# Optimization experiments

Hardware: AMD Instinct MI355X
Metric: run time of the kernel (lower is better)

## Reference

```python
import jax, jax.numpy as jnp
import numpy as np

E = 800_000
D = 64
N_NODES = 50_000


def setup_inputs() -> dict:
    key = jax.random.key(0)
    k1, k2, k3 = jax.random.split(key, 3)
    M = jax.random.normal(k1, (E, D), dtype=jnp.float32)
    edge_index = jax.random.randint(k2, (2, E), 0, N_NODES, dtype=jnp.int64)
    rev_index = jax.random.randint(k3, (E,), 0, E, dtype=jnp.int64)
    return {"M": M, "edge_index": edge_index, "rev_index": rev_index, "dim_size": N_NODES}


def reference(M, edge_index, rev_index, dim_size):
    # directed=True sum-aggregation variant of Aggregation.forward
    src, dest = edge_index[0], edge_index[1]
    # gather: scatter-add edge messages into destination nodes -> [dim_size, D]
    M_v = jax.ops.segment_sum(M, dest, num_segments=dim_size)
    # edge-wise gather by src node, minus reverse-edge message
    return M_v[src] - M[rev_index]
```

## Files before the change

### kernel.cpp

```cpp
#include <hip/hip_runtime.h>


#define D 64
#define N_NODES 50000
#define SCAN_THREADS 1024

__global__ void agg_hist(const int* __restrict__ dest, int* __restrict__ counts, int E) {
    int e = blockIdx.x * blockDim.x + threadIdx.x;
    if (e < E) atomicAdd(counts + dest[e], 1);
}

__global__ void agg_scan(int* __restrict__ data) {
    __shared__ int sums[SCAN_THREADS];
    const int N = N_NODES;
    int t = threadIdx.x;
    const int chunk = (N + SCAN_THREADS - 1) / SCAN_THREADS;
    int start = t * chunk;
    int end   = min(start + chunk, N);
    int s = 0;
    for (int i = start; i < end; ++i) s += data[i];
    sums[t] = s;
    __syncthreads();
    for (int off = 1; off < SCAN_THREADS; off <<= 1) {
        int v = sums[t];
        int u = (t >= off) ? sums[t - off] : 0;
        __syncthreads();
        sums[t] = v + u;
        __syncthreads();
    }
    int run = (t == 0) ? 0 : sums[t - 1];
    for (int i = start; i < end; ++i) {
        int c = data[i];
        data[i] = run;
        run += c;
    }
    if (t == SCAN_THREADS - 1) data[N] = run;
}

__global__ void agg_bin(const int* __restrict__ dest, int* __restrict__ cursor,
                        int* __restrict__ order, int E) {
    int e = blockIdx.x * blockDim.x + threadIdx.x;
    if (e < E) {
        int pos = atomicAdd(cursor + dest[e], 1);
        order[pos] = e;
    }
}

__global__ void agg_reduce(const float* __restrict__ M,
                           const int* __restrict__ order,
                           const int* __restrict__ offsets,
                           float* __restrict__ Mv) {
    int lane = threadIdx.x & 63;
    int node = (blockIdx.x * blockDim.x + threadIdx.x) >> 6;
    if (node >= N_NODES) return;
    int beg = offsets[node];
    int end = offsets[node + 1];
    float acc = 0.f;
    int i = beg;
    for (; i + 4 <= end; i += 4) {
        int e0 = order[i];
        int e1 = order[i + 1];
        int e2 = order[i + 2];
        int e3 = order[i + 3];
        float a0 = M[(size_t)e0 * D + lane];
        float a1 = M[(size_t)e1 * D + lane];
        float a2 = M[(size_t)e2 * D + lane];
        float a3 = M[(size_t)e3 * D + lane];
        acc += (a0 + a1) + (a2 + a3);
    }
    for (; i < end; ++i) acc += M[(size_t)order[i] * D + lane];
    Mv[(size_t)node * D + lane] = acc;
}

__global__ void agg_gather(const float* __restrict__ Mv,
                           const float* __restrict__ M,
                           const int* __restrict__ src,
                           const int* __restrict__ rev,
                           float* __restrict__ out,
                           int E) {
    int gid = blockIdx.x * blockDim.x + threadIdx.x;
    int e  = gid >> 4;
    int c4 = gid & 15;
    if (e >= E) return;
    int s = src[e];
    int r = rev[e];
    float4 a = reinterpret_cast<const float4*>(Mv + (size_t)s * D)[c4];
    float4 b = reinterpret_cast<const float4*>(M  + (size_t)r * D)[c4];
    float4 o;
    o.x = a.x - b.x;
    o.y = a.y - b.y;
    o.z = a.z - b.z;
    o.w = a.w - b.w;
    reinterpret_cast<float4*>(out + (size_t)e * D)[c4] = o;
}

extern "C" void kernel_launch(void* const* d_in, const int* in_sizes, int n_in,
                              void* d_out, int out_size, void* d_ws, size_t ws_size,
                              hipStream_t stream) {
    const float* M   = (const float*)d_in[0];
    const int*   ei  = (const int*)d_in[1];
    const int*   rev = (const int*)d_in[2];

    int E = in_sizes[0] / D;
    const int* src  = ei;
    const int* dest = ei + E;

    int*   offsets = (int*)d_ws;
    int*   cursor  = offsets + 50304;
    int*   order   = cursor + 50304;
    float* Mv      = (float*)(order + 800128);

    hipMemsetAsync(offsets, 0, (N_NODES + 1) * sizeof(int), stream);

    int eb = (E + 255) / 256;
    agg_hist<<<eb, 256, 0, stream>>>(dest, offsets, E);
    agg_scan<<<1, SCAN_THREADS, 0, stream>>>(offsets);
    hipMemcpyAsync(cursor, offsets, (N_NODES + 1) * sizeof(int),
                   hipMemcpyDeviceToDevice, stream);
    agg_bin<<<eb, 256, 0, stream>>>(dest, cursor, order, E);

    int rb = (N_NODES * 64 + 255) / 256;
    agg_reduce<<<rb, 256, 0, stream>>>(M, order, offsets, Mv);

    int gb = (E * 16 + 255) / 256;
    agg_gather<<<gb, 256, 0, stream>>>(Mv, M, src, rev, (float*)d_out, E);
}
```

Measured before the change: 581.5 us.

## Vectorize hist/bin, coalesced warp-shuffle scan writing cursor, unroll reduce, nontemporal stores

The histogram and binning kernels now process four edges per thread using int4 loads. The single-block scan becomes a coalesced, tiled wavefront-shuffle scan that also writes the cursor array, which removes the device-to-device memcpy. The reduce loop is unrolled to eight loads with four independent accumulators to expose more memory-level parallelism. The gather writes its output with nontemporal stores. Together these target launch overhead, the serial uncoalesced scan, and memory latency, at the cost of fewer threads in the atomic kernels and a different floating-point summation order.

```diff
diff --git a/kernel.cpp b/kernel.cpp
--- a/kernel.cpp
+++ b/kernel.cpp
@@ -5,44 +5,73 @@
 #define N_NODES 50000
 #define SCAN_THREADS 1024
 
+typedef float f4 __attribute__((ext_vector_type(4)));
+
 __global__ void agg_hist(const int* __restrict__ dest, int* __restrict__ counts, int E) {
-    int e = blockIdx.x * blockDim.x + threadIdx.x;
-    if (e < E) atomicAdd(counts + dest[e], 1);
+    int t = blockIdx.x * blockDim.x + threadIdx.x;
+    int e = t << 2;
+    if (e + 3 < E) {
+        int4 d = *reinterpret_cast<const int4*>(dest + e);
+        atomicAdd(counts + d.x, 1);
+        atomicAdd(counts + d.y, 1);
+        atomicAdd(counts + d.z, 1);
+        atomicAdd(counts + d.w, 1);
+    } else {
+        for (; e < E; ++e) atomicAdd(counts + dest[e], 1);
+    }
 }
 
-__global__ void agg_scan(int* __restrict__ data) {
-    __shared__ int sums[SCAN_THREADS];
-    const int N = N_NODES;
-    int t = threadIdx.x;
-    const int chunk = (N + SCAN_THREADS - 1) / SCAN_THREADS;
-    int start = t * chunk;
-    int end   = min(start + chunk, N);
-    int s = 0;
-    for (int i = start; i < end; ++i) s += data[i];
-    sums[t] = s;
+__global__ void agg_scan(int* __restrict__ data, int* __restrict__ cursor) {
+    __shared__ int wsums[SCAN_THREADS / 64];
+    __shared__ int carry_sh;
+    const int t = threadIdx.x;
+    const int lane = t & 63;
+    const int w = t >> 6;
+    if (t == 0) carry_sh = 0;
     __syncthreads();
-    for (int off = 1; off < SCAN_THREADS; off <<= 1) {
-        int v = sums[t];
-        int u = (t >= off) ? sums[t - off] : 0;
+    for (int base = 0; base < N_NODES; base += SCAN_THREADS) {
+        int i = base + t;
+        int v = (i < N_NODES) ? data[i] : 0;
+        int carry = carry_sh;
+        int x = v;
+        #pragma unroll
+        for (int off = 1; off < 64; off <<= 1) {
+            int y = __shfl_up(x, off, 64);
+            if (lane >= off) x += y;
+        }
+        if (lane == 63) wsums[w] = x;
         __syncthreads();
-        sums[t] = v + u;
+        if (t == 0) {
+            int run = 0;
+            #pragma unroll
+            for (int k = 0; k < SCAN_THREADS / 64; ++k) {
+                int c = wsums[k]; wsums[k] = run; run += c;
+            }
+            carry_sh = carry + run;
+        }
+        __syncthreads();
+        int excl = carry + wsums[w] + (x - v);
+        if (i < N_NODES) { data[i] = excl; cursor[i] = excl; }
         __syncthreads();
     }
-    int run = (t == 0) ? 0 : sums[t - 1];
-    for (int i = start; i < end; ++i) {
-        int c = data[i];
-        data[i] = run;
-        run += c;
-    }
-    if (t == SCAN_THREADS - 1) data[N] = run;
+    if (t == 0) { data[N_NODES] = carry_sh; cursor[N_NODES] = carry_sh; }
 }
 
 __global__ void agg_bin(const int* __restrict__ dest, int* __restrict__ cursor,
                         int* __restrict__ order, int E) {
-    int e = blockIdx.x * blockDim.x + threadIdx.x;
-    if (e < E) {
-        int pos = atomicAdd(cursor + dest[e], 1);
-        order[pos] = e;
+    int t = blockIdx.x * blockDim.x + threadIdx.x;
+    int e = t << 2;
+    if (e + 3 < E) {
+        int4 d = *reinterpret_cast<const int4*>(dest + e);
+        int p0 = atomicAdd(cursor + d.x, 1); order[p0] = e;
+        int p1 = atomicAdd(cursor + d.y, 1); order[p1] = e + 1;
+        int p2 = atomicAdd(cursor + d.z, 1); order[p2] = e + 2;
+        int p3 = atomicAdd(cursor + d.w, 1); order[p3] = e + 3;
+    } else {
+        for (; e < E; ++e) {
+            int pos = atomicAdd(cursor + dest[e], 1);
+            order[pos] = e;
+        }
     }
 }
 
@@ -55,21 +84,26 @@
     if (node >= N_NODES) return;
     int beg = offsets[node];
     int end = offsets[node + 1];
-    float acc = 0.f;
+    float acc0 = 0.f, acc1 = 0.f, acc2 = 0.f, acc3 = 0.f;
     int i = beg;
-    for (; i + 4 <= end; i += 4) {
-        int e0 = order[i];
-        int e1 = order[i + 1];
-        int e2 = order[i + 2];
-        int e3 = order[i + 3];
+    for (; i + 8 <= end; i += 8) {
+        int e0 = order[i + 0], e1 = order[i + 1], e2 = order[i + 2], e3 = order[i + 3];
+        int e4 = order[i + 4], e5 = order[i + 5], e6 = order[i + 6], e7 = order[i + 7];
         float a0 = M[(size_t)e0 * D + lane];
         float a1 = M[(size_t)e1 * D + lane];
         float a2 = M[(size_t)e2 * D + lane];
         float a3 = M[(size_t)e3 * D + lane];
-        acc += (a0 + a1) + (a2 + a3);
+        float a4 = M[(size_t)e4 * D + lane];
+        float a5 = M[(size_t)e5 * D + lane];
+        float a6 = M[(size_t)e6 * D + lane];
+        float a7 = M[(size_t)e7 * D + lane];
+        acc0 += a0 + a4;
+        acc1 += a1 + a5;
+        acc2 += a2 + a6;
+        acc3 += a3 + a7;
     }
-    for (; i < end; ++i) acc += M[(size_t)order[i] * D + lane];
-    Mv[(size_t)node * D + lane] = acc;
+    for (; i < end; ++i) acc0 += M[(size_t)order[i] * D + lane];
+    Mv[(size_t)node * D + lane] = (acc0 + acc1) + (acc2 + acc3);
 }
 
 __global__ void agg_gather(const float* __restrict__ Mv,
@@ -84,14 +118,10 @@
     if (e >= E) return;
     int s = src[e];
     int r = rev[e];
-    float4 a = reinterpret_cast<const float4*>(Mv + (size_t)s * D)[c4];
-    float4 b = reinterpret_cast<const float4*>(M  + (size_t)r * D)[c4];
-    float4 o;
-    o.x = a.x - b.x;
-    o.y = a.y - b.y;
-    o.z = a.z - b.z;
-    o.w = a.w - b.w;
-    reinterpret_cast<float4*>(out + (size_t)e * D)[c4] = o;
+    f4 a = reinterpret_cast<const f4*>(Mv + (size_t)s * D)[c4];
+    f4 b = reinterpret_cast<const f4*>(M  + (size_t)r * D)[c4];
+    f4 o = a - b;
+    __builtin_nontemporal_store(o, reinterpret_cast<f4*>(out + (size_t)e * D) + c4);
 }
 
 extern "C" void kernel_launch(void* const* d_in, const int* in_sizes, int n_in,
@@ -112,12 +142,10 @@
 
     hipMemsetAsync(offsets, 0, (N_NODES + 1) * sizeof(int), stream);
 
-    int eb = (E + 255) / 256;
-    agg_hist<<<eb, 256, 0, stream>>>(dest, offsets, E);
-    agg_scan<<<1, SCAN_THREADS, 0, stream>>>(offsets);
-    hipMemcpyAsync(cursor, offsets, (N_NODES + 1) * sizeof(int),
-                   hipMemcpyDeviceToDevice, stream);
-    agg_bin<<<eb, 256, 0, stream>>>(dest, cursor, order, E);
+    int hb = ((E + 3) / 4 + 255) / 256;
+    agg_hist<<<hb, 256, 0, stream>>>(dest, offsets, E);
+    agg_scan<<<1, SCAN_THREADS, 0, stream>>>(offsets, cursor);
+    agg_bin<<<hb, 256, 0, stream>>>(dest, cursor, order, E);
 
     int rb = (N_NODES * 64 + 255) / 256;
     agg_reduce<<<rb, 256, 0, stream>>>(M, order, offsets, Mv);
```

Result: faster. 539.8 us (-7.2%).
